# Performance work log

Measured on AMD Instinct MI355X. Metric: run time of the kernel, lower is better.

The kernel has to match this reference:

```python
import jax, jax.numpy as jnp
import numpy as np
import math

B, IN_DIM, HID, OUT_DIM = 8192, 64, 256, 4096
N_STEPS = 20


def logx_and_kl(loga, logb, alpha):
    # logx = log(alpha*a + (1-alpha)*b); kl = KL(x || b)
    logx = jnp.logaddexp(loga + jnp.log(alpha), logb + jnp.log(1.0 - alpha))
    kl = jnp.sum(jnp.exp(logx) * (logx - logb), axis=-1, keepdims=True)
    return logx, kl


def dkl_dalpha(loga, logb, logx):
    a_minus_b = jnp.exp(loga) - jnp.exp(logb)
    return jnp.sum(a_minus_b * (logx - logb + 1.0), axis=-1, keepdims=True)


def findalphafork(loga, logb, k, n_steps=N_STEPS):
    def body(i, carry):
        alpha, bot, top = carry
        logx, kl = logx_and_kl(loga, logb, alpha)
        bot = jnp.where(k >= kl, alpha, bot)
        top = jnp.where(k <= kl, alpha, top)
        d = dkl_dalpha(loga, logb, logx)
        delta = (k - kl) / (d + 1e-12)
        alpha = jnp.clip(alpha + delta,
                         bot * (15.0 / 16.0) + top * (1.0 / 16.0),
                         bot * 0.5 + top * 0.5)
        return alpha, bot, top

    init = (jnp.ones_like(k), jnp.zeros_like(k), jnp.ones_like(k))
    alpha, _, _ = jax.lax.fori_loop(0, n_steps, body, init)
    return alpha


def kl_fixed_mixture(k, loga, logb):
    alpha = findalphafork(loga, logb, k)
    return logx_and_kl(loga, logb, alpha)


def setup_inputs() -> dict:
    key = jax.random.key(0)
    ks = jax.random.split(key, 10)
    x = jax.random.normal(ks[0], (B, IN_DIM), dtype=jnp.float32)
    kl_budget = jax.random.uniform(ks[1], (B, 1), dtype=jnp.float32)
    log_base_dist = jax.nn.log_softmax(
        jax.random.normal(ks[2], (B, OUT_DIM), dtype=jnp.float32), axis=-1)
    W0 = jax.random.normal(ks[3], (HID, IN_DIM + 1), dtype=jnp.float32) * (0.05 / math.sqrt(IN_DIM + 1))
    b0 = jax.random.normal(ks[4], (HID,), dtype=jnp.float32) * 0.01
    W1 = jax.random.normal(ks[5], (HID, HID), dtype=jnp.float32) * (1.0 / math.sqrt(HID))
    b1 = jax.random.normal(ks[6], (HID,), dtype=jnp.float32) * 0.01
    W2 = jax.random.normal(ks[7], (OUT_DIM + 1, HID), dtype=jnp.float32) * 0.01
    b2 = jax.random.normal(ks[8], (OUT_DIM + 1,), dtype=jnp.float32) * 0.01
    return {"x": x, "kl_budget": kl_budget, "log_base_dist": log_base_dist,
            "W0": W0, "b0": b0, "W1": W1, "b1": b1, "W2": W2, "b2": b2,
            "actions_left": 16}


def reference(x, kl_budget, log_base_dist, W0, b0, W1, b1, W2, b2, actions_left):
    h = jnp.concatenate([x, kl_budget], axis=-1)  # [B, IN_DIM+1]
    for i, (W, b) in enumerate(((W0, b0), (W1, b1), (W2, b2))):
        if i != 0:
            h = jnp.tanh(h)
        h = h @ W.T + b
    # n_versions_last_layer == 1 -> selected_x = h
    kl_target = jax.nn.sigmoid(h[:, :1] - math.log(actions_left)) * kl_budget + 1e-6
    loga = h[:, 1:] + log_base_dist
    loga = loga - jnp.max(loga, axis=-1, keepdims=True)
    loga = loga - jax.nn.logsumexp(loga, axis=-1, keepdims=True)
    logx, kl_achieved = kl_fixed_mixture(kl_target, loga, log_base_dist)
    return jax.nn.softmax(logx, axis=-1), jnp.square(kl_achieved - kl_target)
```

## Files before the change

kernel.cpp:

```cpp
#include <hip/hip_runtime.h>
#include <hip/hip_bf16.h>
#include <math.h>

typedef float f32x4 __attribute__((ext_vector_type(4)));
typedef __bf16 bf16x8 __attribute__((ext_vector_type(8)));
typedef _Float16 f16;
typedef _Float16 f16x4 __attribute__((ext_vector_type(4)));
typedef unsigned short ushort;

#define NROWS 8192
#define HID 256
#define NCOL 4096
#define NSTEPS 20

static __device__ inline float bf2f(ushort u) {
    union { unsigned int i; float f; } c; c.i = ((unsigned int)u) << 16; return c.f;
}
static __device__ inline ushort f2bf(float x) {
    __hip_bfloat16 h = __float2bfloat16(x);
    union { __hip_bfloat16 h; ushort u; } c; c.h = h; return c.u;
}
static __device__ inline float fast_tanh(float x) {
    float e = __expf(2.0f * x);
    return 1.0f - 2.0f / (e + 1.0f);
}
static __device__ inline void gload_lds16(const void* g, void* l) {
    __builtin_amdgcn_global_load_lds(
        (const __attribute__((address_space(1))) void*)g,
        (__attribute__((address_space(3))) void*)l, 16, 0, 0);
}

__global__ __launch_bounds__(256) void prep_kernel(
    const float* __restrict__ W2, const float* __restrict__ b2,
    const float* __restrict__ W0, const float* __restrict__ W1,
    ushort* __restrict__ Bext, float* __restrict__ b2s,
    float* __restrict__ W0t, float* __restrict__ W1t)
{
    const int r = blockIdx.x, t = threadIdx.x;
    Bext[(size_t)r * 256 + t] = f2bf(W2[(size_t)(r + 1) * 256 + t]);
    if (t == 0) b2s[r] = b2[r + 1];
    if (r < 256) W1t[r * 256 + t] = W1[t * 256 + r];
    if (r < 65)  W0t[r * 256 + t] = W0[t * 65 + r];
}

__global__ __launch_bounds__(256) void mlp01_kernel(
    const float* __restrict__ x, const float* __restrict__ klb,
    const float* __restrict__ W0t, const float* __restrict__ b0,
    const float* __restrict__ W1t, const float* __restrict__ b1,
    const float* __restrict__ W2, const float* __restrict__ b2,
    const int* __restrict__ AL,
    ushort* __restrict__ t_ext, float* __restrict__ kt)
{
    __shared__ float xk[16][66];
    __shared__ float h0[16][HID];
    __shared__ float ktred[16][4];
    const int tid = threadIdx.x;
    const int lane = tid & 63, w = tid >> 6;
    const int r0 = blockIdx.x * 16;

    for (int f = tid; f < 16 * 64; f += 256) {
        int r = f >> 6, k = f & 63;
        xk[r][k] = x[(size_t)(r0 + r) * 64 + k];
    }
    if (tid < 16) xk[tid][64] = klb[r0 + tid];
    __syncthreads();

    {
        float acc[16];
        float bb = b0[tid];
        #pragma unroll
        for (int r = 0; r < 16; r++) acc[r] = bb;
        for (int k = 0; k < 65; k++) {
            float wv = W0t[k * 256 + tid];
            #pragma unroll
            for (int r = 0; r < 16; r++) acc[r] = fmaf(wv, xk[r][k], acc[r]);
        }
        #pragma unroll
        for (int r = 0; r < 16; r++) h0[r][tid] = fast_tanh(acc[r]);
    }
    __syncthreads();
    {
        float acc[16];
        float bb = b1[tid];
        #pragma unroll
        for (int r = 0; r < 16; r++) acc[r] = bb;
        for (int k = 0; k < HID; k++) {
            float wv = W1t[k * 256 + tid];
            #pragma unroll
            for (int r = 0; r < 16; r++) acc[r] = fmaf(wv, h0[r][k], acc[r]);
        }
        const float w2v = W2[tid];
        __syncthreads();
        #pragma unroll
        for (int r = 0; r < 16; r++) {
            float v = fast_tanh(acc[r]);
            t_ext[(size_t)(r0 + r) * 256 + tid] = f2bf(v);
            float p = v * w2v;
            #pragma unroll
            for (int off = 1; off < 64; off <<= 1) p += __shfl_xor(p, off);
            if (lane == 0) ktred[r][w] = p;
        }
        __syncthreads();
        if (tid < 16) {
            float accv = ktred[tid][0] + ktred[tid][1] + ktred[tid][2] + ktred[tid][3];
            float z = accv + b2[0] - logf((float)AL[0]);
            float sg = 1.0f / (1.0f + expf(-z));
            kt[r0 + tid] = sg * klb[r0 + tid] + 1e-6f;
        }
    }
}

__global__ __launch_bounds__(256) void gemm2_mfma(
    const ushort* __restrict__ Aext, const ushort* __restrict__ Bext,
    const float* __restrict__ b2s, f16* __restrict__ h2f)
{
    __shared__ ushort As[128 * 64];
    __shared__ ushort Bs[128 * 64];
    const int tid = threadIdx.x;
    const int lane = tid & 63, w = tid >> 6;
    const int bid = blockIdx.y * 32 + blockIdx.x;
    const int swz = (bid & 7) * 256 + (bid >> 3);
    const int m0 = (swz >> 5) * 128, c0 = (swz & 31) * 128;
    const int wm = w & 1, wn = w >> 1;

    f32x4 acc[4][4];
    #pragma unroll
    for (int i = 0; i < 4; i++)
        #pragma unroll
        for (int j = 0; j < 4; j++) acc[i][j] = (f32x4){0.f, 0.f, 0.f, 0.f};

    int sg_row[4], sg_c[4];
    #pragma unroll
    for (int s = 0; s < 4; s++) {
        int idx = (s * 4 + w) * 512 + lane * 8;
        int row = idx >> 6;
        int cp = (idx >> 3) & 7;
        sg_row[s] = row;
        sg_c[s] = cp ^ (row & 7);
    }

    for (int kt = 0; kt < 4; kt++) {
        const int k0 = kt * 64;
        #pragma unroll
        for (int s = 0; s < 4; s++) {
            gload_lds16(&Aext[(size_t)(m0 + sg_row[s]) * 256 + k0 + sg_c[s] * 8],
                        &As[(s * 4 + w) * 512]);
            gload_lds16(&Bext[(size_t)(c0 + sg_row[s]) * 256 + k0 + sg_c[s] * 8],
                        &Bs[(s * 4 + w) * 512]);
        }
        __syncthreads();
        #pragma unroll
        for (int kk = 0; kk < 2; kk++) {
            const int cA = kk * 4 + (lane >> 4);
            bf16x8 af[4], bfr[4];
            #pragma unroll
            for (int i = 0; i < 4; i++) {
                int mr = wm * 64 + i * 16 + (lane & 15);
                af[i] = *(const bf16x8*)&As[mr * 64 + ((cA ^ (mr & 7)) * 8)];
                int nr = wn * 64 + i * 16 + (lane & 15);
                bfr[i] = *(const bf16x8*)&Bs[nr * 64 + ((cA ^ (nr & 7)) * 8)];
            }
            #pragma unroll
            for (int i = 0; i < 4; i++)
                #pragma unroll
                for (int j = 0; j < 4; j++)
                    acc[i][j] = __builtin_amdgcn_mfma_f32_16x16x32_bf16(
                        af[i], bfr[j], acc[i][j], 0, 0, 0);
        }
        __syncthreads();
    }

    const int colb = c0 + wn * 64 + (lane & 15);
    #pragma unroll
    for (int j = 0; j < 4; j++) {
        float bias = b2s[colb + j * 16];
        #pragma unroll
        for (int i = 0; i < 4; i++) {
            int rr = m0 + wm * 64 + i * 16 + (lane >> 4) * 4;
            #pragma unroll
            for (int q = 0; q < 4; q++)
                h2f[(size_t)(rr + q) * 4096 + colb + j * 16] = (f16)(acc[i][j][q] + bias);
        }
    }
}

__global__ __launch_bounds__(256) void solve256(
    float* __restrict__ out, const f16* __restrict__ h2f,
    const float* __restrict__ logb, const float* __restrict__ ktarr)
{
    __shared__ float red[16];
    const int tid = threadIdx.x;
    const int lane = tid & 63, w = tid >> 6;
    const int r = blockIdx.x;

    const f16* hrow = h2f + (size_t)r * 4096;
    const float* brow = logb + (size_t)r * 4096;

    f16x4 h4[4];
    f32x4 bv4[4];
    #pragma unroll
    for (int c = 0; c < 4; c++) {
        h4[c] = *(const f16x4*)&hrow[c * 1024 + tid * 4];
        bv4[c] = *(const f32x4*)&brow[c * 1024 + tid * 4];
    }

    float e[16];
    float s = 0.0f, sav = 0.0f;
    #pragma unroll
    for (int c = 0; c < 4; c++)
        #pragma unroll
        for (int j = 0; j < 4; j++) {
            int m = c * 4 + j;
            float av = (float)h4[c][j];
            e[m] = __expf(av + bv4[c][j]);
            s += e[m];
            sav = fmaf(e[m], av, sav);
        }
    #pragma unroll
    for (int off = 1; off < 64; off <<= 1) {
        s   += __shfl_xor(s, off);
        sav += __shfl_xor(sav, off);
    }
    if (lane == 0) { red[w * 2] = s; red[w * 2 + 1] = sav; }
    __syncthreads();
    s   = red[0] + red[2] + red[4] + red[6];
    sav = red[1] + red[3] + red[5] + red[7];

    const float k = ktarr[r];
    const float lns = __logf(s);
    const float inv = 1.0f / s;
    const float kl1 = fmaf(sav, inv, -lns);

    float* orow = out + (size_t)r * 4096;

    if (k >= kl1) {
        #pragma unroll
        for (int c = 0; c < 4; c++) {
            f32x4 o;
            #pragma unroll
            for (int j = 0; j < 4; j++) o[j] = e[c * 4 + j] * inv;
            *(f32x4*)&orow[c * 1024 + tid * 4] = o;
        }
        if (tid == 0) {
            float d = kl1 - k;
            out[(size_t)NROWS * NCOL + r] = d * d;
        }
        return;
    }

    float eb[16];
    float c2 = 0.0f, c3 = 0.0f, seb = 0.0f, samv = 0.0f;
    #pragma unroll
    for (int c = 0; c < 4; c++)
        #pragma unroll
        for (int j = 0; j < 4; j++) {
            int m = c * 4 + j;
            float b = bv4[c][j];
            float ebv = __expf(b);
            eb[m] = ebv;
            float a = fmaf(e[m], inv, -ebv);
            float av = (float)h4[c][j];
            e[m] = a;
            c2  = fmaf(ebv, b, c2);
            c3  = fmaf(a, b, c3);
            seb += ebv;
            samv = fmaf(a, av, samv);
        }
    #pragma unroll
    for (int off = 1; off < 64; off <<= 1) {
        c2   += __shfl_xor(c2, off);
        c3   += __shfl_xor(c3, off);
        seb  += __shfl_xor(seb, off);
        samv += __shfl_xor(samv, off);
    }
    __syncthreads();
    if (lane == 0) {
        red[w * 4 + 0] = c2;  red[w * 4 + 1] = c3;
        red[w * 4 + 2] = seb; red[w * 4 + 3] = samv;
    }
    __syncthreads();
    c2   = red[0] + red[4] + red[8]  + red[12];
    c3   = red[1] + red[5] + red[9]  + red[13];
    seb  = red[2] + red[6] + red[10] + red[14];
    samv = red[3] + red[7] + red[11] + red[15];

    const float C2 = c2;
    const float C3 = c3;
    const float C4 = (1.0f - seb) - C3;

    float skl = kl1, a_eval = 1.0f;
    float bot = 0.0f, top = 1.0f;
    float d1 = samv - lns * (1.0f - seb) + C4;
    float alpha = fminf(0.5f, fmaxf(1.0f / 16.0f,
                        1.0f + (k - kl1) / (d1 + 1e-12f)));

    for (int it = 1; it < NSTEPS; it++) {
        a_eval = alpha;
        float kacc = 0.0f, dacc = 0.0f;
        #pragma unroll
        for (int m = 0; m < 16; m++) {
            float xv = fmaf(alpha, e[m], eb[m]);
            float lx = __logf(xv);
            kacc = fmaf(xv, lx, kacc);
            dacc = fmaf(e[m], lx, dacc);
        }
        #pragma unroll
        for (int off = 1; off < 64; off <<= 1) {
            kacc += __shfl_xor(kacc, off);
            dacc += __shfl_xor(dacc, off);
        }
        __syncthreads();
        if (lane == 0) { red[w * 2 + 0] = kacc; red[w * 2 + 1] = dacc; }
        __syncthreads();
        kacc = red[0] + red[2] + red[4] + red[6];
        dacc = red[1] + red[3] + red[5] + red[7];

        float klc = kacc - C2 - alpha * C3;
        float dc  = dacc + C4;
        skl = klc;

        bot = (k >= klc) ? alpha : bot;
        top = (k <= klc) ? alpha : top;
        float delta = (k - klc) / (dc + 1e-12f);
        float lo = bot * (15.0f / 16.0f) + top * (1.0f / 16.0f);
        float hi = 0.5f * (bot + top);
        alpha = fminf(hi, fmaxf(lo, alpha + delta));
        if (top - bot < 1e-6f) break;
    }

    if (alpha != a_eval) {
        float kacc = 0.0f;
        #pragma unroll
        for (int m = 0; m < 16; m++) {
            float xv = fmaf(alpha, e[m], eb[m]);
            kacc = fmaf(xv, __logf(xv), kacc);
        }
        #pragma unroll
        for (int off = 1; off < 64; off <<= 1) kacc += __shfl_xor(kacc, off);
        __syncthreads();
        if (lane == 0) red[w] = kacc;
        __syncthreads();
        kacc = red[0] + red[1] + red[2] + red[3];
        skl = kacc - C2 - alpha * C3;
    }

    const float spx = fmaf(alpha, 1.0f - seb, seb);
    const float invs = 1.0f / spx;
    #pragma unroll
    for (int c = 0; c < 4; c++) {
        f32x4 o;
        #pragma unroll
        for (int j = 0; j < 4; j++)
            o[j] = fmaf(alpha, e[c * 4 + j], eb[c * 4 + j]) * invs;
        *(f32x4*)&orow[c * 1024 + tid * 4] = o;
    }
    if (tid == 0) {
        float d = skl - k;
        out[(size_t)NROWS * NCOL + r] = d * d;
    }
}

extern "C" void kernel_launch(void* const* d_in, const int* in_sizes, int n_in,
                              void* d_out, int out_size, void* d_ws, size_t ws_size,
                              hipStream_t stream)
{
    const float* x    = (const float*)d_in[0];
    const float* klb  = (const float*)d_in[1];
    const float* logb = (const float*)d_in[2];
    const float* W0   = (const float*)d_in[3];
    const float* b0   = (const float*)d_in[4];
    const float* W1   = (const float*)d_in[5];
    const float* b1   = (const float*)d_in[6];
    const float* W2   = (const float*)d_in[7];
    const float* b2   = (const float*)d_in[8];
    const int*   AL   = (const int*)d_in[9];
    float* out = (float*)d_out;

    const size_t MB = 1048576ull;
    const size_t KB = 1024ull;
    char* p = (char*)d_ws;
    ushort* tws  = (ushort*)(p);
    ushort* Bext = (ushort*)(p + 4 * MB);
    float*  kt   = (float*) (p + 6 * MB);
    float*  b2s  = (float*) (p + 6 * MB + 64 * KB);
    float*  W0t  = (float*) (p + 6 * MB + 128 * KB);
    float*  W1t  = (float*) (p + 6 * MB + 256 * KB);
    f16*    h2f  = (f16*)   (p + 8 * MB);

    hipLaunchKernelGGL(prep_kernel, dim3(4096), dim3(256), 0, stream,
                       W2, b2, W0, W1, Bext, b2s, W0t, W1t);
    hipLaunchKernelGGL(mlp01_kernel, dim3(512), dim3(256), 0, stream,
                       x, klb, W0t, b0, W1t, b1, W2, b2, AL, tws, kt);
    hipLaunchKernelGGL(gemm2_mfma, dim3(32, 64), dim3(256), 0, stream, tws, Bext, b2s, h2f);
    hipLaunchKernelGGL(solve256, dim3(8192), dim3(256), 0, stream, out, h2f, logb, kt);
}
```

Before: 157.1 us.

## Split solver into fast early-exit kernel and flagged slow Newton kernel

Rows where the full-mixture KL already fits the budget are handled by a compact 4-rows-per-block kernel that writes softmax directly, and other rows are flagged. A second kernel runs the iterative alpha search only for flagged rows, exiting immediately otherwise. This separates the light path from the register-heavy iterative path to improve occupancy, at the cost of an extra launch and re-reading inputs for slow rows.

```diff
diff --git a/kernel.cpp b/kernel.cpp
--- a/kernel.cpp
+++ b/kernel.cpp
@@ -184,14 +184,18 @@
     }
 }
 
-__global__ __launch_bounds__(256) void solve256(
+__global__ __launch_bounds__(1024) void solve_fast(
     float* __restrict__ out, const f16* __restrict__ h2f,
-    const float* __restrict__ logb, const float* __restrict__ ktarr)
-{
-    __shared__ float red[16];
+    const float* __restrict__ logb, const float* __restrict__ ktarr,
+    unsigned char* __restrict__ flag)
+{
+    __shared__ float red[32];
     const int tid = threadIdx.x;
-    const int lane = tid & 63, w = tid >> 6;
-    const int r = blockIdx.x;
+    const int lane = tid & 63;
+    const int gw = tid >> 6;
+    const int row = tid >> 8;
+    const int t = tid & 255;
+    const int r = blockIdx.x * 4 + row;
 
     const f16* hrow = h2f + (size_t)r * 4096;
     const float* brow = logb + (size_t)r * 4096;
@@ -200,8 +204,8 @@
     f32x4 bv4[4];
     #pragma unroll
     for (int c = 0; c < 4; c++) {
-        h4[c] = *(const f16x4*)&hrow[c * 1024 + tid * 4];
-        bv4[c] = *(const f32x4*)&brow[c * 1024 + tid * 4];
+        h4[c] = *(const f16x4*)&hrow[c * 1024 + t * 4];
+        bv4[c] = *(const f32x4*)&brow[c * 1024 + t * 4];
     }
 
     float e[16];
@@ -221,32 +225,84 @@
         s   += __shfl_xor(s, off);
         sav += __shfl_xor(sav, off);
     }
-    if (lane == 0) { red[w * 2] = s; red[w * 2 + 1] = sav; }
-    __syncthreads();
-    s   = red[0] + red[2] + red[4] + red[6];
-    sav = red[1] + red[3] + red[5] + red[7];
+    if (lane == 0) { red[gw * 2] = s; red[gw * 2 + 1] = sav; }
+    __syncthreads();
+    s   = red[row * 8 + 0] + red[row * 8 + 2] + red[row * 8 + 4] + red[row * 8 + 6];
+    sav = red[row * 8 + 1] + red[row * 8 + 3] + red[row * 8 + 5] + red[row * 8 + 7];
 
     const float k = ktarr[r];
     const float lns = __logf(s);
     const float inv = 1.0f / s;
     const float kl1 = fmaf(sav, inv, -lns);
 
-    float* orow = out + (size_t)r * 4096;
-
     if (k >= kl1) {
+        if (t == 0) flag[r] = 0;
+        float* orow = out + (size_t)r * 4096;
         #pragma unroll
         for (int c = 0; c < 4; c++) {
             f32x4 o;
             #pragma unroll
             for (int j = 0; j < 4; j++) o[j] = e[c * 4 + j] * inv;
-            *(f32x4*)&orow[c * 1024 + tid * 4] = o;
-        }
-        if (tid == 0) {
+            *(f32x4*)&orow[c * 1024 + t * 4] = o;
+        }
+        if (t == 0) {
             float d = kl1 - k;
             out[(size_t)NROWS * NCOL + r] = d * d;
         }
-        return;
-    }
+    } else {
+        if (t == 0) flag[r] = 1;
+    }
+}
+
+__global__ __launch_bounds__(256) void solve_slow(
+    float* __restrict__ out, const f16* __restrict__ h2f,
+    const float* __restrict__ logb, const float* __restrict__ ktarr,
+    const unsigned char* __restrict__ flag)
+{
+    __shared__ float red[16];
+    const int r = blockIdx.x;
+    if (!flag[r]) return;
+    const int tid = threadIdx.x;
+    const int lane = tid & 63, w = tid >> 6;
+
+    const f16* hrow = h2f + (size_t)r * 4096;
+    const float* brow = logb + (size_t)r * 4096;
+
+    f16x4 h4[4];
+    f32x4 bv4[4];
+    #pragma unroll
+    for (int c = 0; c < 4; c++) {
+        h4[c] = *(const f16x4*)&hrow[c * 1024 + tid * 4];
+        bv4[c] = *(const f32x4*)&brow[c * 1024 + tid * 4];
+    }
+
+    float e[16];
+    float s = 0.0f, sav = 0.0f;
+    #pragma unroll
+    for (int c = 0; c < 4; c++)
+        #pragma unroll
+        for (int j = 0; j < 4; j++) {
+            int m = c * 4 + j;
+            float av = (float)h4[c][j];
+            e[m] = __expf(av + bv4[c][j]);
+            s += e[m];
+            sav = fmaf(e[m], av, sav);
+        }
+    #pragma unroll
+    for (int off = 1; off < 64; off <<= 1) {
+        s   += __shfl_xor(s, off);
+        sav += __shfl_xor(sav, off);
+    }
+    if (lane == 0) { red[w * 2] = s; red[w * 2 + 1] = sav; }
+    __syncthreads();
+    s   = red[0] + red[2] + red[4] + red[6];
+    sav = red[1] + red[3] + red[5] + red[7];
+
+    const float k = ktarr[r];
+    const float lns = __logf(s);
+    const float inv = 1.0f / s;
+    const float kl1 = fmaf(sav, inv, -lns);
+    float* orow = out + (size_t)r * 4096;
 
     float eb[16];
     float c2 = 0.0f, c3 = 0.0f, seb = 0.0f, samv = 0.0f;
@@ -385,6 +441,7 @@
     float*  b2s  = (float*) (p + 6 * MB + 64 * KB);
     float*  W0t  = (float*) (p + 6 * MB + 128 * KB);
     float*  W1t  = (float*) (p + 6 * MB + 256 * KB);
+    unsigned char* flag = (unsigned char*)(p + 7 * MB);
     f16*    h2f  = (f16*)   (p + 8 * MB);
 
     hipLaunchKernelGGL(prep_kernel, dim3(4096), dim3(256), 0, stream,
@@ -392,5 +449,6 @@
     hipLaunchKernelGGL(mlp01_kernel, dim3(512), dim3(256), 0, stream,
                        x, klb, W0t, b0, W1t, b1, W2, b2, AL, tws, kt);
     hipLaunchKernelGGL(gemm2_mfma, dim3(32, 64), dim3(256), 0, stream, tws, Bext, b2s, h2f);
-    hipLaunchKernelGGL(solve256, dim3(8192), dim3(256), 0, stream, out, h2f, logb, kt);
-}
+    hipLaunchKernelGGL(solve_fast, dim3(2048), dim3(1024), 0, stream, out, h2f, logb, kt, flag);
+    hipLaunchKernelGGL(solve_slow, dim3(8192), dim3(256), 0, stream, out, h2f, logb, kt, flag);
+}
```

After: 172.7 us. 1.1x slower.

## Pack four rows per 1024-thread block in the mixture solver kernel

Applied to the files above, without the earlier changes.

The solver kernel now processes four rows per block of 1024 threads instead of one row per 256-thread block. Shared bitmasks track which rows need the iterative solve and which have converged, so the loop continues until every slow row in the block is done. This cuts block count and launch/scheduling overhead, but rows in a block now move in lockstep. A fast row can therefore wait on a slow neighbour, and the larger blocks add more barriers.

```diff
diff --git a/kernel.cpp b/kernel.cpp
--- a/kernel.cpp
+++ b/kernel.cpp
@@ -184,14 +184,21 @@
     }
 }
 
-__global__ __launch_bounds__(256) void solve256(
+__global__ __launch_bounds__(1024) void solve4(
     float* __restrict__ out, const f16* __restrict__ h2f,
     const float* __restrict__ logb, const float* __restrict__ ktarr)
 {
-    __shared__ float red[16];
+    __shared__ float red[32];
+    __shared__ int slowmask;
+    __shared__ int donemask;
     const int tid = threadIdx.x;
-    const int lane = tid & 63, w = tid >> 6;
-    const int r = blockIdx.x;
+    const int lane = tid & 63;
+    const int gw = tid >> 6;
+    const int row = tid >> 8;
+    const int t = tid & 255;
+    const int r = blockIdx.x * 4 + row;
+
+    if (tid == 0) { slowmask = 0; donemask = 0; }
 
     const f16* hrow = h2f + (size_t)r * 4096;
     const float* brow = logb + (size_t)r * 4096;
@@ -200,8 +207,8 @@
     f32x4 bv4[4];
     #pragma unroll
     for (int c = 0; c < 4; c++) {
-        h4[c] = *(const f16x4*)&hrow[c * 1024 + tid * 4];
-        bv4[c] = *(const f32x4*)&brow[c * 1024 + tid * 4];
+        h4[c] = *(const f16x4*)&hrow[c * 1024 + t * 4];
+        bv4[c] = *(const f32x4*)&brow[c * 1024 + t * 4];
     }
 
     float e[16];
@@ -221,32 +228,36 @@
         s   += __shfl_xor(s, off);
         sav += __shfl_xor(sav, off);
     }
-    if (lane == 0) { red[w * 2] = s; red[w * 2 + 1] = sav; }
-    __syncthreads();
-    s   = red[0] + red[2] + red[4] + red[6];
-    sav = red[1] + red[3] + red[5] + red[7];
+    if (lane == 0) { red[gw * 2] = s; red[gw * 2 + 1] = sav; }
+    __syncthreads();
+    s   = red[row * 8 + 0] + red[row * 8 + 2] + red[row * 8 + 4] + red[row * 8 + 6];
+    sav = red[row * 8 + 1] + red[row * 8 + 3] + red[row * 8 + 5] + red[row * 8 + 7];
 
     const float k = ktarr[r];
     const float lns = __logf(s);
     const float inv = 1.0f / s;
     const float kl1 = fmaf(sav, inv, -lns);
 
+    const bool slow = (k < kl1);
     float* orow = out + (size_t)r * 4096;
 
-    if (k >= kl1) {
+    if (!slow) {
         #pragma unroll
         for (int c = 0; c < 4; c++) {
             f32x4 o;
             #pragma unroll
             for (int j = 0; j < 4; j++) o[j] = e[c * 4 + j] * inv;
-            *(f32x4*)&orow[c * 1024 + tid * 4] = o;
-        }
-        if (tid == 0) {
+            *(f32x4*)&orow[c * 1024 + t * 4] = o;
+        }
+        if (t == 0) {
             float d = kl1 - k;
             out[(size_t)NROWS * NCOL + r] = d * d;
         }
-        return;
-    }
+    } else if (t == 0) {
+        atomicOr(&slowmask, 1 << row);
+    }
+    __syncthreads();
+    if (slowmask == 0) return;
 
     float eb[16];
     float c2 = 0.0f, c3 = 0.0f, seb = 0.0f, samv = 0.0f;
@@ -275,14 +286,20 @@
     }
     __syncthreads();
     if (lane == 0) {
-        red[w * 4 + 0] = c2;  red[w * 4 + 1] = c3;
-        red[w * 4 + 2] = seb; red[w * 4 + 3] = samv;
-    }
-    __syncthreads();
-    c2   = red[0] + red[4] + red[8]  + red[12];
-    c3   = red[1] + red[5] + red[9]  + red[13];
-    seb  = red[2] + red[6] + red[10] + red[14];
-    samv = red[3] + red[7] + red[11] + red[15];
+        red[gw * 2 + 0] = c2;
+        red[gw * 2 + 1] = c3;
+    }
+    __syncthreads();
+    c2 = red[row * 8 + 0] + red[row * 8 + 2] + red[row * 8 + 4] + red[row * 8 + 6];
+    c3 = red[row * 8 + 1] + red[row * 8 + 3] + red[row * 8 + 5] + red[row * 8 + 7];
+    __syncthreads();
+    if (lane == 0) {
+        red[gw * 2 + 0] = seb;
+        red[gw * 2 + 1] = samv;
+    }
+    __syncthreads();
+    seb  = red[row * 8 + 0] + red[row * 8 + 2] + red[row * 8 + 4] + red[row * 8 + 6];
+    samv = red[row * 8 + 1] + red[row * 8 + 3] + red[row * 8 + 5] + red[row * 8 + 7];
 
     const float C2 = c2;
     const float C3 = c3;
@@ -295,7 +312,8 @@
                         1.0f + (k - kl1) / (d1 + 1e-12f)));
 
     for (int it = 1; it < NSTEPS; it++) {
-        a_eval = alpha;
+        const bool rowdone = ((donemask >> row) & 1) || !slow;
+        a_eval = rowdone ? a_eval : alpha;
         float kacc = 0.0f, dacc = 0.0f;
         #pragma unroll
         for (int m = 0; m < 16; m++) {
@@ -310,25 +328,29 @@
             dacc += __shfl_xor(dacc, off);
         }
         __syncthreads();
-        if (lane == 0) { red[w * 2 + 0] = kacc; red[w * 2 + 1] = dacc; }
-        __syncthreads();
-        kacc = red[0] + red[2] + red[4] + red[6];
-        dacc = red[1] + red[3] + red[5] + red[7];
-
-        float klc = kacc - C2 - alpha * C3;
-        float dc  = dacc + C4;
-        skl = klc;
-
-        bot = (k >= klc) ? alpha : bot;
-        top = (k <= klc) ? alpha : top;
-        float delta = (k - klc) / (dc + 1e-12f);
-        float lo = bot * (15.0f / 16.0f) + top * (1.0f / 16.0f);
-        float hi = 0.5f * (bot + top);
-        alpha = fminf(hi, fmaxf(lo, alpha + delta));
-        if (top - bot < 1e-6f) break;
-    }
-
-    if (alpha != a_eval) {
+        if (lane == 0) { red[gw * 2 + 0] = kacc; red[gw * 2 + 1] = dacc; }
+        __syncthreads();
+        kacc = red[row * 8 + 0] + red[row * 8 + 2] + red[row * 8 + 4] + red[row * 8 + 6];
+        dacc = red[row * 8 + 1] + red[row * 8 + 3] + red[row * 8 + 5] + red[row * 8 + 7];
+
+        if (!rowdone) {
+            float klc = kacc - C2 - alpha * C3;
+            float dc  = dacc + C4;
+            skl = klc;
+            bot = (k >= klc) ? alpha : bot;
+            top = (k <= klc) ? alpha : top;
+            float delta = (k - klc) / (dc + 1e-12f);
+            float lo = bot * (15.0f / 16.0f) + top * (1.0f / 16.0f);
+            float hi = 0.5f * (bot + top);
+            alpha = fminf(hi, fmaxf(lo, alpha + delta));
+            if (t == 0 && (top - bot < 1e-6f))
+                atomicOr(&donemask, 1 << row);
+        }
+        __syncthreads();
+        if ((donemask | ~slowmask) == ~0) break;
+    }
+
+    {
         float kacc = 0.0f;
         #pragma unroll
         for (int m = 0; m < 16; m++) {
@@ -338,25 +360,27 @@
         #pragma unroll
         for (int off = 1; off < 64; off <<= 1) kacc += __shfl_xor(kacc, off);
         __syncthreads();
-        if (lane == 0) red[w] = kacc;
-        __syncthreads();
-        kacc = red[0] + red[1] + red[2] + red[3];
-        skl = kacc - C2 - alpha * C3;
-    }
-
-    const float spx = fmaf(alpha, 1.0f - seb, seb);
-    const float invs = 1.0f / spx;
-    #pragma unroll
-    for (int c = 0; c < 4; c++) {
-        f32x4 o;
-        #pragma unroll
-        for (int j = 0; j < 4; j++)
-            o[j] = fmaf(alpha, e[c * 4 + j], eb[c * 4 + j]) * invs;
-        *(f32x4*)&orow[c * 1024 + tid * 4] = o;
-    }
-    if (tid == 0) {
-        float d = skl - k;
-        out[(size_t)NROWS * NCOL + r] = d * d;
+        if (lane == 0) red[gw] = kacc;
+        __syncthreads();
+        kacc = red[row * 4 + 0] + red[row * 4 + 1] + red[row * 4 + 2] + red[row * 4 + 3];
+        if (alpha != a_eval) skl = kacc - C2 - alpha * C3;
+    }
+
+    if (slow) {
+        const float spx = fmaf(alpha, 1.0f - seb, seb);
+        const float invs = 1.0f / spx;
+        #pragma unroll
+        for (int c = 0; c < 4; c++) {
+            f32x4 o;
+            #pragma unroll
+            for (int j = 0; j < 4; j++)
+                o[j] = fmaf(alpha, e[c * 4 + j], eb[c * 4 + j]) * invs;
+            *(f32x4*)&orow[c * 1024 + t * 4] = o;
+        }
+        if (t == 0) {
+            float d = skl - k;
+            out[(size_t)NROWS * NCOL + r] = d * d;
+        }
     }
 }
 
@@ -392,5 +416,5 @@
     hipLaunchKernelGGL(mlp01_kernel, dim3(512), dim3(256), 0, stream,
                        x, klb, W0t, b0, W1t, b1, W2, b2, AL, tws, kt);
     hipLaunchKernelGGL(gemm2_mfma, dim3(32, 64), dim3(256), 0, stream, tws, Bext, b2s, h2f);
-    hipLaunchKernelGGL(solve256, dim3(8192), dim3(256), 0, stream, out, h2f, logb, kt);
-}
+    hipLaunchKernelGGL(solve4, dim3(2048), dim3(1024), 0, stream, out, h2f, logb, kt);
+}
```

Measured after the change: 185.3 us. 1.18x slower.
